# Kernel tuning notes

Hardware: AMD Instinct MI355X
Metric: run time of the kernel (lower is better)

## Reference

```python
import jax, jax.numpy as jnp
import numpy as np

B, T, DIM = 64, 1024, 64
HID = 5 * DIM          # MADE hidden width
NOUT = 2 * DIM         # (s, t) concatenated


def _build_masks(nin, hidden_sizes, nout, seed=0):
    """MADE connectivity masks, returned in weight layout (out_features, in_features)."""
    rng = np.random.RandomState(seed)
    m = {-1: np.arange(nin)}  # natural ordering
    L = len(hidden_sizes)
    for l in range(L):
        m[l] = rng.randint(m[l - 1].min(), nin - 1, size=hidden_sizes[l])
    masks = [m[l - 1][:, None] <= m[l][None, :] for l in range(L)]
    masks.append(m[L - 1][:, None] < m[-1][None, :])
    k = nout // nin
    masks[-1] = np.concatenate([masks[-1]] * k, axis=1)
    return [jnp.asarray(msk.T.astype(np.float32)) for msk in masks]


def _xavier(key, out_f, in_f):
    lim = np.sqrt(6.0 / (in_f + out_f)).astype(np.float32)
    return jax.random.uniform(key, (out_f, in_f), jnp.float32, -lim, lim)


def setup_inputs() -> dict:
    key = jax.random.key(0)
    kz, k1, k2, k3 = jax.random.split(key, 4)
    M1, M2, M3 = _build_masks(DIM, [HID, HID], NOUT, seed=0)
    return {
        "z": jax.random.normal(kz, (B, T, DIM), jnp.float32),
        "W1": _xavier(k1, HID, DIM),  "b1": jnp.zeros((HID,), jnp.float32),
        "W2": _xavier(k2, HID, HID),  "b2": jnp.zeros((HID,), jnp.float32),
        "W3": _xavier(k3, NOUT, HID), "b3": jnp.zeros((NOUT,), jnp.float32),
        "M1": M1, "M2": M2, "M3": M3,
    }


def reference(z, W1, b1, W2, b2, W3, b3, M1, M2, M3):
    dim = z.shape[-1]
    mw1, mw2, mw3 = M1 * W1, M2 * W2, M3 * W3  # masked weights, (out,in)

    def made(x):  # x: [B,T,dim] -> st: [B,T,2*dim]
        h = jax.nn.relu(jnp.einsum("btd,hd->bth", x, mw1) + b1)
        h = jax.nn.relu(jnp.einsum("bth,gh->btg", h, mw2) + b2)
        return jnp.einsum("btg,og->bto", h, mw3) + b3

    zf = z[:, :, ::-1]  # parity=True flip along feature dim

    def step(carry, i):
        x, log_det = carry
        st = made(x)
        s, t = st[..., :dim], st[..., dim:]
        si = s[:, :, i]
        xi = (zf[:, :, i] - t[:, :, i]) * jnp.exp(-si)
        x = x.at[:, :, i].set(xi)
        return (x, log_det - si), None

    x0 = jnp.zeros_like(z)
    ld0 = jnp.zeros(z.shape[:2], z.dtype)
    (x, log_det), _ = jax.lax.scan(step, (x0, ld0), jnp.arange(dim))

    # NaN replacement (deterministic RNG) + clamp, matching torch.where chains
    kx, kl = jax.random.split(jax.random.key(1))
    x = jnp.where(jnp.isnan(x), jax.random.normal(kx, x.shape, x.dtype), x)
    log_det = jnp.where(jnp.isnan(log_det), jax.random.normal(kl, log_det.shape, log_det.dtype), log_det)
    x = jnp.clip(x, -100.0, 100.0)
    log_det = jnp.clip(log_det, -100.0, 100.0)
    return x, log_det
```

## Files before the change

kernel.cpp:

```cpp
#include <hip/hip_runtime.h>
#include <math.h>

#define HIDN 320
#define DIMN 64

#define W1T_OFF 0
#define W2T_OFF 20480
#define W3I_OFF 122880
#define B1P_OFF 163840
#define B2P_OFF 164160
#define FTOT    164480

__global__ __launch_bounds__(320) void maf_setup(const float* __restrict__ M1,
                                                 const float* __restrict__ M3,
                                                 int* __restrict__ wsi) {
  __shared__ int m0[HIDN], m1[HIDN];
  __shared__ int c1[64], c2[64];
  __shared__ int s1[65], s2[65];
  int t = threadIdx.x;
  if (t < 64) { c1[t] = 0; c2[t] = 0; }
  __syncthreads();
  if (t < HIDN) {
    float s = 0.f;
    for (int d = 0; d < DIMN; ++d) s += M1[t * DIMN + d];
    int a = (int)(s + 0.5f) - 1;
    m0[t] = a;
    atomicAdd(&c1[a], 1);
    float sb = 0.f;
    for (int o = 0; o < DIMN; ++o) sb += M3[o * HIDN + t];
    int b = 63 - (int)(sb + 0.5f);
    m1[t] = b;
    atomicAdd(&c2[b], 1);
  }
  __syncthreads();
  if (t == 0) {
    int a = 0;
    for (int v = 0; v < 64; ++v) { s1[v] = a; a += c1[v]; }
    s1[64] = a;
    a = 0;
    for (int v = 0; v < 64; ++v) { s2[v] = a; a += c2[v]; }
    s2[64] = a;
  }
  __syncthreads();
  if (t < HIDN) {
    int key = m0[t], rk = 0;
    for (int h = 0; h < t; ++h) rk += (m0[h] == key);
    wsi[s1[key] + rk] = t;
    int key2 = m1[t], rk2 = 0;
    for (int g = 0; g < t; ++g) rk2 += (m1[g] == key2);
    wsi[320 + s2[key2] + rk2] = t;
  }
  if (t < 65) { wsi[640 + t] = s1[t]; wsi[705 + t] = s2[t]; }
}

__global__ void maf_fill(const float* __restrict__ W1, const float* __restrict__ b1,
                         const float* __restrict__ W2, const float* __restrict__ b2,
                         const float* __restrict__ W3,
                         const float* __restrict__ M1, const float* __restrict__ M2,
                         const float* __restrict__ M3,
                         const int* __restrict__ wsi, float* __restrict__ wsf) {
  int idx = blockIdx.x * blockDim.x + threadIdx.x;
  const int* p1 = wsi;
  const int* p2 = wsi + 320;
  if (idx < 20480) {
    int i = idx / 320, hp = idx % 320;
    int h = p1[hp];
    wsf[W1T_OFF + idx] = M1[h * 64 + i] * W1[h * 64 + i];
  } else if (idx < 122880) {
    int e = idx - 20480;
    int hp = e / 320, gp = e % 320;
    int h = p1[hp], g = p2[gp];
    wsf[idx] = M2[g * 320 + h] * W2[g * 320 + h];
  } else if (idx < 163840) {
    int e = idx - 122880;
    int c = e & 1, q = e >> 1;
    int i = q / 320, gp = q % 320;
    int g = p2[gp];
    int row = i + (c ? 64 : 0);
    wsf[idx] = M3[row * 320 + g] * W3[row * 320 + g];
  } else if (idx < 164160) {
    wsf[idx] = b1[p1[idx - 163840]];
  } else if (idx < 164480) {
    wsf[idx] = b2[p2[idx - 164160]];
  }
}

#define RWS 16
#define H1S 328

__global__ __launch_bounds__(256, 4) void maf_main(
    const float* __restrict__ z, const float* __restrict__ b3,
    const float* __restrict__ wsf, const int* __restrict__ wsi,
    float* __restrict__ out) {
  __shared__ float h1p[RWS * H1S];
  __shared__ float zr[RWS * 64];
  __shared__ float xv[RWS * 64];
  __shared__ int s1[65], s2[65];

  const int tid = threadIdx.x;
  const int r = tid >> 4;
  const int j = tid & 15;
  const long long bt0 = (long long)blockIdx.x * RWS;

  const float* b1p = wsf + B1P_OFF;
  const float* b2p = wsf + B2P_OFF;

  for (int rr = 0; rr < RWS; ++rr)
    for (int c = tid; c < HIDN; c += 256)
      h1p[rr * H1S + c] = b1p[c];

  for (int k = tid; k < RWS * 64; k += 256) {
    int rr = k >> 6, c = k & 63;
    zr[k] = z[(bt0 + rr) * 64 + (63 - c)];
  }
  if (tid < 65) { s1[tid] = wsi[640 + tid]; s2[tid] = wsi[705 + tid]; }

  float h2[20];
#pragma unroll
  for (int k = 0; k < 20; ++k) h2[k] = b2p[j + 16 * k];

  float logdet = 0.f;

  for (int i = 0; i < 64; ++i) {
    __syncthreads();
    const int p = s2[i];

    float ss = 0.f, tt = 0.f;
    const float* w3row = wsf + W3I_OFF + i * 640;
#pragma unroll
    for (int k = 0; k < 20; ++k) {
      int g = j + 16 * k;
      if (g < p) {
        float v = fmaxf(h2[k], 0.f);
        float2 w = *reinterpret_cast<const float2*>(w3row + 2 * g);
        ss = fmaf(w.x, v, ss);
        tt = fmaf(w.y, v, tt);
      }
    }
#pragma unroll
    for (int m = 1; m < 16; m <<= 1) {
      ss += __shfl_xor(ss, m);
      tt += __shfl_xor(tt, m);
    }
    ss += b3[i];
    tt += b3[64 + i];
    const float xi = (zr[(r << 6) + i] - tt) * expf(-ss);
    logdet -= ss;
    if (j == 0) xv[(r << 6) + i] = xi;

    const int h0 = s1[i], h1e = s1[i + 1];
    const float* w1row = wsf + W1T_OFF + i * HIDN;
    for (int hb = h0; hb < h1e; hb += 8) {
      float av[8];
#pragma unroll
      for (int u = 0; u < 8; ++u) {
        int hp = hb + u;
        int hpc = hp < h1e ? hp : h1e - 1;
        float a = fmaf(w1row[hpc], xi, h1p[r * H1S + hpc]);
        av[u] = (hp < h1e) ? fmaxf(a, 0.f) : 0.f;
      }
#pragma unroll
      for (int k = 0; k < 20; ++k) {
        int g = j + 16 * k;
        if (g >= p) {
          float acc = h2[k];
#pragma unroll
          for (int u = 0; u < 8; ++u) {
            int hp = hb + u;
            int hpc = hp < h1e ? hp : h1e - 1;
            acc = fmaf(wsf[W2T_OFF + hpc * HIDN + g], av[u], acc);
          }
          h2[k] = acc;
        }
      }
    }

    for (int hp = s1[i + 1] + j; hp < HIDN; hp += 16) {
      h1p[r * H1S + hp] = fmaf(w1row[hp], xi, h1p[r * H1S + hp]);
    }
  }

  __syncthreads();
  for (int k = tid; k < RWS * 64; k += 256) {
    float v = xv[k];
    v = fminf(fmaxf(v, -100.f), 100.f);
    out[bt0 * 64 + k] = v;
  }
  if (j == 0) {
    float v = fminf(fmaxf(logdet, -100.f), 100.f);
    out[4194304LL + bt0 + r] = v;
  }
}

extern "C" void kernel_launch(void* const* d_in, const int* in_sizes, int n_in,
                              void* d_out, int out_size, void* d_ws, size_t ws_size,
                              hipStream_t stream) {
  const float* z  = (const float*)d_in[0];
  const float* W1 = (const float*)d_in[1];
  const float* b1 = (const float*)d_in[2];
  const float* W2 = (const float*)d_in[3];
  const float* b2 = (const float*)d_in[4];
  const float* W3 = (const float*)d_in[5];
  const float* b3 = (const float*)d_in[6];
  const float* M1 = (const float*)d_in[7];
  const float* M2 = (const float*)d_in[8];
  const float* M3 = (const float*)d_in[9];
  float* out = (float*)d_out;
  float* wsf = (float*)d_ws;
  int* wsi = (int*)((char*)d_ws + (size_t)FTOT * sizeof(float));

  if (ws_size < (size_t)FTOT * sizeof(float) + 770 * sizeof(int)) return;

  maf_setup<<<1, 320, 0, stream>>>(M1, M3, wsi);
  maf_fill<<<(164480 + 255) / 256, 256, 0, stream>>>(W1, b1, W2, b2, W3, M1, M2, M3, wsi, wsf);
  maf_main<<<4096, 256, 0, stream>>>(z, b3, wsf, wsi, out);
}
```

Before: 1.715 ms.

## Transpose W2 layout, vectorize loads, drop per-step block barriers in MAF kernel

Stores the permuted masked W2 with the output index as the major dimension, so each thread reads 8 contiguous hidden weights as two float4 loads instead of eight strided scalar loads. Each 16-thread row group now owns its own h1 row and z/x buffer, which removes the per-iteration __syncthreads and the extra xv buffer. Loop bounds become wave-uniform via readfirstlane, predicates become selects, and expf becomes __expf. Occupancy hint rises to 5 blocks. The cost is some wasted FMAs on masked lanes, extra register pressure under the tighter launch bound, and a fast-math exp.

```diff
diff --git a/kernel.cpp b/kernel.cpp
--- a/kernel.cpp
+++ b/kernel.cpp
@@ -68,7 +68,7 @@
     wsf[W1T_OFF + idx] = M1[h * 64 + i] * W1[h * 64 + i];
   } else if (idx < 122880) {
     int e = idx - 20480;
-    int hp = e / 320, gp = e % 320;
+    int gp = e / 320, hp = e % 320;
     int h = p1[hp], g = p2[gp];
     wsf[idx] = M2[g * 320 + h] * W2[g * 320 + h];
   } else if (idx < 163840) {
@@ -88,14 +88,13 @@
 #define RWS 16
 #define H1S 328
 
-__global__ __launch_bounds__(256, 4) void maf_main(
+__global__ __launch_bounds__(256, 5) void maf_main(
     const float* __restrict__ z, const float* __restrict__ b3,
     const float* __restrict__ wsf, const int* __restrict__ wsi,
     float* __restrict__ out) {
   __shared__ float h1p[RWS * H1S];
-  __shared__ float zr[RWS * 64];
-  __shared__ float xv[RWS * 64];
-  __shared__ int s1[65], s2[65];
+  __shared__ float zx[RWS * 64];
+  __shared__ int s1s[65], s2s[65];
 
   const int tid = threadIdx.x;
   const int r = tid >> 4;
@@ -104,16 +103,16 @@
 
   const float* b1p = wsf + B1P_OFF;
   const float* b2p = wsf + B2P_OFF;
-
-  for (int rr = 0; rr < RWS; ++rr)
-    for (int c = tid; c < HIDN; c += 256)
-      h1p[rr * H1S + c] = b1p[c];
+  float* h1r = h1p + r * H1S;
+
+  for (int c = j; c < HIDN; c += 16) h1r[c] = b1p[c];
 
   for (int k = tid; k < RWS * 64; k += 256) {
     int rr = k >> 6, c = k & 63;
-    zr[k] = z[(bt0 + rr) * 64 + (63 - c)];
-  }
-  if (tid < 65) { s1[tid] = wsi[640 + tid]; s2[tid] = wsi[705 + tid]; }
+    zx[k] = z[(bt0 + rr) * 64 + (63 - c)];
+  }
+  if (tid < 65) { s1s[tid] = wsi[640 + tid]; s2s[tid] = wsi[705 + tid]; }
+  __syncthreads();
 
   float h2[20];
 #pragma unroll
@@ -122,16 +121,19 @@
   float logdet = 0.f;
 
   for (int i = 0; i < 64; ++i) {
-    __syncthreads();
-    const int p = s2[i];
+    const int p   = __builtin_amdgcn_readfirstlane(s2s[i]);
+    const int h0  = __builtin_amdgcn_readfirstlane(s1s[i]);
+    const int h1e = __builtin_amdgcn_readfirstlane(s1s[i + 1]);
 
     float ss = 0.f, tt = 0.f;
     const float* w3row = wsf + W3I_OFF + i * 640;
+    const int keg = (p + 15) >> 4;
 #pragma unroll
     for (int k = 0; k < 20; ++k) {
-      int g = j + 16 * k;
-      if (g < p) {
+      if (k < keg) {
+        int g = j + 16 * k;
         float v = fmaxf(h2[k], 0.f);
+        v = (g < p) ? v : 0.f;
         float2 w = *reinterpret_cast<const float2*>(w3row + 2 * g);
         ss = fmaf(w.x, v, ss);
         tt = fmaf(w.y, v, tt);
@@ -144,47 +146,68 @@
     }
     ss += b3[i];
     tt += b3[64 + i];
-    const float xi = (zr[(r << 6) + i] - tt) * expf(-ss);
+    const float xi = (zx[(r << 6) + i] - tt) * __expf(-ss);
     logdet -= ss;
-    if (j == 0) xv[(r << 6) + i] = xi;
-
-    const int h0 = s1[i], h1e = s1[i + 1];
+    zx[(r << 6) + i] = xi;
+
     const float* w1row = wsf + W1T_OFF + i * HIDN;
-    for (int hb = h0; hb < h1e; hb += 8) {
+    const int hb0 = h0 & ~7;
+    const int k0 = p >> 4;
+    for (int hb = hb0; hb < h1e; hb += 8) {
+      float4 ha = *reinterpret_cast<const float4*>(&h1r[hb]);
+      float4 hb4 = *reinterpret_cast<const float4*>(&h1r[hb + 4]);
+      float4 wa = *reinterpret_cast<const float4*>(w1row + hb);
+      float4 wb = *reinterpret_cast<const float4*>(w1row + hb + 4);
       float av[8];
-#pragma unroll
-      for (int u = 0; u < 8; ++u) {
-        int hp = hb + u;
-        int hpc = hp < h1e ? hp : h1e - 1;
-        float a = fmaf(w1row[hpc], xi, h1p[r * H1S + hpc]);
-        av[u] = (hp < h1e) ? fmaxf(a, 0.f) : 0.f;
+      {
+        float hv[8] = {ha.x, ha.y, ha.z, ha.w, hb4.x, hb4.y, hb4.z, hb4.w};
+        float wv[8] = {wa.x, wa.y, wa.z, wa.w, wb.x, wb.y, wb.z, wb.w};
+#pragma unroll
+        for (int u = 0; u < 8; ++u) {
+          int hp = hb + u;
+          float a = fmaf(wv[u], xi, hv[u]);
+          av[u] = (hp >= h0 && hp < h1e) ? fmaxf(a, 0.f) : 0.f;
+        }
       }
 #pragma unroll
       for (int k = 0; k < 20; ++k) {
-        int g = j + 16 * k;
-        if (g >= p) {
+        if (k >= k0) {
+          int g = j + 16 * k;
+          const float* w2g = wsf + W2T_OFF + g * HIDN + hb;
+          float4 qa = *reinterpret_cast<const float4*>(w2g);
+          float4 qb = *reinterpret_cast<const float4*>(w2g + 4);
           float acc = h2[k];
-#pragma unroll
-          for (int u = 0; u < 8; ++u) {
-            int hp = hb + u;
-            int hpc = hp < h1e ? hp : h1e - 1;
-            acc = fmaf(wsf[W2T_OFF + hpc * HIDN + g], av[u], acc);
-          }
-          h2[k] = acc;
+          acc = fmaf(qa.x, av[0], acc);
+          acc = fmaf(qa.y, av[1], acc);
+          acc = fmaf(qa.z, av[2], acc);
+          acc = fmaf(qa.w, av[3], acc);
+          acc = fmaf(qb.x, av[4], acc);
+          acc = fmaf(qb.y, av[5], acc);
+          acc = fmaf(qb.z, av[6], acc);
+          acc = fmaf(qb.w, av[7], acc);
+          h2[k] = (g >= p) ? acc : h2[k];
         }
       }
     }
 
-    for (int hp = s1[i + 1] + j; hp < HIDN; hp += 16) {
-      h1p[r * H1S + hp] = fmaf(w1row[hp], xi, h1p[r * H1S + hp]);
-    }
-  }
-
-  __syncthreads();
-  for (int k = tid; k < RWS * 64; k += 256) {
-    float v = xv[k];
+    const int ku = h1e >> 4;
+#pragma unroll
+    for (int k = 0; k < 20; ++k) {
+      if (k >= ku) {
+        int hp = j + 16 * k;
+        if (hp >= h1e) {
+          h1r[hp] = fmaf(w1row[hp], xi, h1r[hp]);
+        }
+      }
+    }
+  }
+
+#pragma unroll
+  for (int u = 0; u < 4; ++u) {
+    int c = j + 16 * u;
+    float v = zx[(r << 6) + c];
     v = fminf(fmaxf(v, -100.f), 100.f);
-    out[bt0 * 64 + k] = v;
+    out[(bt0 + r) * 64 + c] = v;
   }
   if (j == 0) {
     float v = fminf(fmaxf(logdet, -100.f), 100.f);
```

New measurement: 4.538 ms. +164.6%, slower.
